# Kernel tuning notes

Measured on AMD Instinct MI355X. Metric: run time of the kernel, lower is better.

The kernel has to match this reference:

```python
import jax, jax.numpy as jnp
import numpy as np

INPUT, HIDDEN, CLASSES = 28, 128, 10

def setup_inputs() -> dict:
    key = jax.random.key(0)
    ks = jax.random.split(key, 8)
    B = 16384
    s_ih = 1.0 / np.sqrt(HIDDEN)
    return {
        "x": jax.random.normal(ks[0], (B, 1, 28, 28), dtype=jnp.float32),
        "W_ih": jax.random.uniform(ks[1], (HIDDEN, INPUT), jnp.float32, -s_ih, s_ih),
        "W_hh": jax.random.uniform(ks[2], (HIDDEN, HIDDEN), jnp.float32, -s_ih, s_ih),
        "b_ih": jax.random.uniform(ks[3], (HIDDEN,), jnp.float32, -s_ih, s_ih),
        "b_hh": jax.random.uniform(ks[4], (HIDDEN,), jnp.float32, -s_ih, s_ih),
        "W_fc": jax.random.uniform(ks[5], (CLASSES, HIDDEN), jnp.float32, -s_ih, s_ih),
        "b_fc": jax.random.uniform(ks[6], (CLASSES,), jnp.float32, -s_ih, s_ih),
    }

def reference(x, W_ih, W_hh, b_ih, b_hh, W_fc, b_fc):
    # x: [B,1,28,28] -> squeeze channel -> [B,T=28,I=28]
    xs = jnp.squeeze(x, axis=1)
    B = xs.shape[0]
    # precompute input projections for all timesteps: [B,T,H]
    xproj = jnp.einsum("bti,hi->bth", xs, W_ih) + b_ih + b_hh
    xproj_t = jnp.transpose(xproj, (1, 0, 2))  # [T,B,H]

    def step(h, xp):
        h_new = jnp.tanh(xp + h @ W_hh.T)
        return h_new, None

    h0 = jnp.zeros((B, HIDDEN), dtype=xs.dtype)
    h_last, _ = jax.lax.scan(step, h0, xproj_t)
    return h_last @ W_fc.T + b_fc  # [B, num_classes]
```

## Files before the change

### kernel.cpp

```cpp
#include <hip/hip_runtime.h>
#include <hip/hip_bf16.h>
#include <stdint.h>


typedef __attribute__((ext_vector_type(8))) short short8;
typedef __attribute__((ext_vector_type(4))) float f32x4;
typedef __attribute__((ext_vector_type(4))) uint32_t u32x4;

union Frag { short8 s; uint32_t u[4]; u32x4 v; };

#define MFMA16(a,b,c) __builtin_amdgcn_mfma_f32_16x16x32_bf16((a),(b),(c),0,0,0)

__device__ __forceinline__ uint32_t pk2(float a, float b){
    union { __hip_bfloat162 h; uint32_t u; } cv;
    cv.h = __float22bfloat162_rn(make_float2(a,b));
    return cv.u;
}
__device__ __forceinline__ float lo16f(uint32_t u){ return __builtin_bit_cast(float, u<<16); }
__device__ __forceinline__ float hi16f(uint32_t u){ return __builtin_bit_cast(float, u & 0xffff0000u); }

__device__ __forceinline__ void cvt8(const f32x4& a, const f32x4& b, Frag& hi, Frag& lo){
    float v[8];
    #pragma unroll
    for(int i=0;i<4;i++){ v[i]=a[i]; v[4+i]=b[i]; }
    #pragma unroll
    for(int q=0;q<4;q++){
        uint32_t h = pk2(v[2*q], v[2*q+1]);
        hi.u[q] = h;
        lo.u[q] = pk2(v[2*q]-lo16f(h), v[2*q+1]-hi16f(h));
    }
}

__device__ __forceinline__ int piperm(int p){
    int jt = p>>4, c = p&15;
    return 32*(jt>>1) + 8*(c>>2) + 4*(jt&1) + (c&3);
}

__device__ __forceinline__ float fast_tanh(float x){
    x = fminf(fmaxf(x, -30.f), 30.f);
    float e = __expf(2.f*x);
    return (e-1.f)*__builtin_amdgcn_rcpf(e+1.f);
}

__global__ __launch_bounds__(256,2) void rnn_fused4(
    const float* __restrict__ x,   const float* __restrict__ Wih,
    const float* __restrict__ Whh, const float* __restrict__ bih,
    const float* __restrict__ bhh, const float* __restrict__ Wfc,
    const float* __restrict__ bfc, float* __restrict__ out)
{
    const int tid  = threadIdx.x;
    const int w    = tid >> 6;
    const int lane = tid & 63;
    const int g = lane>>4, c = lane&15;
    const int b0 = blockIdx.x*16;
    const f32x4 zero4 = {0.f,0.f,0.f,0.f};

    __shared__ uint32_t lds[2][2][4][64][4];

    Frag whh_h[2][4], whh_l[2][4];
    #pragma unroll
    for(int j=0;j<2;j++){
        const int row = piperm(16*(2*w+j) + c);
        const float* rp = Whh + row*128;
        #pragma unroll
        for(int kt=0;kt<4;kt++){
            f32x4 a = *(const f32x4*)(rp + kt*32 + 8*g);
            f32x4 b = *(const f32x4*)(rp + kt*32 + 8*g + 4);
            cvt8(a, b, whh_h[j][kt], whh_l[j][kt]);
        }
    }

    Frag wih_h[2], wih_l[2];
    {
        const int i1 = 8*g;
        const int i2 = (g<3) ? (8*g+4) : 24;
        #pragma unroll
        for(int j=0;j<2;j++){
            const int row = piperm(16*(2*w+j) + c);
            const float* rp = Wih + row*28;
            f32x4 a = *(const f32x4*)(rp + i1);
            f32x4 b = *(const f32x4*)(rp + i2);
            if (g==3) b = zero4;
            cvt8(a, b, wih_h[j], wih_l[j]);
        }
    }

    f32x4 biasr[2];
    #pragma unroll
    for(int j=0;j<2;j++){
        #pragma unroll
        for(int r=0;r<4;r++){
            int q = piperm(16*(2*w+j) + 4*g + r);
            biasr[j][r] = bih[q] + bhh[q];
        }
    }

    Frag bh_h[4], bh_l[4];
    #pragma unroll
    for(int kt=0;kt<4;kt++){
        #pragma unroll
        for(int q=0;q<4;q++){ bh_h[kt].u[q]=0; bh_l[kt].u[q]=0; }
    }

    const float* xrow = x + (size_t)(b0 + c)*784;
    const int o1 = 8*g;
    const int o2 = (g<3) ? (8*g+4) : 24;

    f32x4 xA = *(const f32x4*)(xrow + o1);
    f32x4 xB = *(const f32x4*)(xrow + o2);

    for(int t=0; t<28; ++t){
        f32x4 xA_n = xA, xB_n = xB;
        if (t < 27){
            xA_n = *(const f32x4*)(xrow + (t+1)*28 + o1);
            xB_n = *(const f32x4*)(xrow + (t+1)*28 + o2);
        }
        Frag bx_h, bx_l;
        {
            f32x4 b = xB;
            if (g==3) b = zero4;
            cvt8(xA, b, bx_h, bx_l);
        }
        f32x4 acc[2];
        #pragma unroll
        for(int j=0;j<2;j++){
            f32x4 a1 = MFMA16(wih_h[j].s, bx_h.s, biasr[j]);
            a1 = MFMA16(wih_l[j].s, bx_h.s, a1);
            a1 = MFMA16(wih_h[j].s, bx_l.s, a1);
            a1 = MFMA16(whh_h[j][0].s, bh_h[0].s, a1);
            a1 = MFMA16(whh_l[j][0].s, bh_h[0].s, a1);
            a1 = MFMA16(whh_h[j][0].s, bh_l[0].s, a1);
            a1 = MFMA16(whh_h[j][1].s, bh_h[1].s, a1);
            a1 = MFMA16(whh_l[j][1].s, bh_h[1].s, a1);
            a1 = MFMA16(whh_h[j][1].s, bh_l[1].s, a1);
            f32x4 a2 = MFMA16(whh_h[j][2].s, bh_h[2].s, zero4);
            a2 = MFMA16(whh_l[j][2].s, bh_h[2].s, a2);
            a2 = MFMA16(whh_h[j][2].s, bh_l[2].s, a2);
            a2 = MFMA16(whh_h[j][3].s, bh_h[3].s, a2);
            a2 = MFMA16(whh_l[j][3].s, bh_h[3].s, a2);
            a2 = MFMA16(whh_h[j][3].s, bh_l[3].s, a2);
            acc[j] = a1 + a2;
        }
        Frag nh_h, nh_l;
        #pragma unroll
        for(int j=0;j<2;j++){
            float h0 = fast_tanh(acc[j][0]);
            float h1 = fast_tanh(acc[j][1]);
            float h2 = fast_tanh(acc[j][2]);
            float h3 = fast_tanh(acc[j][3]);
            const int q0 = j*2;
            uint32_t u0 = pk2(h0,h1), u1 = pk2(h2,h3);
            nh_h.u[q0]   = u0;
            nh_h.u[q0+1] = u1;
            nh_l.u[q0]   = pk2(h0-lo16f(u0), h1-hi16f(u0));
            nh_l.u[q0+1] = pk2(h2-lo16f(u1), h3-hi16f(u1));
        }
        const int buf = t & 1;
        *(u32x4*)(&lds[buf][0][w][lane][0]) = nh_h.v;
        *(u32x4*)(&lds[buf][1][w][lane][0]) = nh_l.v;
        __syncthreads();
        #pragma unroll
        for(int kt=0;kt<4;kt++){
            bh_h[kt].v = *(const u32x4*)(&lds[buf][0][kt][lane][0]);
            bh_l[kt].v = *(const u32x4*)(&lds[buf][1][kt][lane][0]);
        }
        xA = xA_n; xB = xB_n;
    }

    if (w == 0){
        Frag wfc_h[4], wfc_l[4];
        const bool valid = (c < 10);
        const float* rp = Wfc + (valid ? c : 0)*128;
        #pragma unroll
        for(int kt=0;kt<4;kt++){
            f32x4 a = *(const f32x4*)(rp + kt*32 + 8*g);
            f32x4 b = *(const f32x4*)(rp + kt*32 + 8*g + 4);
            if(!valid){ a = zero4; b = zero4; }
            cvt8(a, b, wfc_h[kt], wfc_l[kt]);
        }
        f32x4 accf = {0.f,0.f,0.f,0.f};
        #pragma unroll
        for(int kt=0;kt<4;kt++){
            accf = MFMA16(wfc_h[kt].s, bh_h[kt].s, accf);
            accf = MFMA16(wfc_l[kt].s, bh_h[kt].s, accf);
            accf = MFMA16(wfc_h[kt].s, bh_l[kt].s, accf);
        }
        #pragma unroll
        for(int r=0;r<4;r++){
            int cls = 4*g + r;
            if (cls < 10){
                out[(size_t)(b0+c)*10 + cls] = accf[r] + bfc[cls];
            }
        }
    }
}

extern "C" void kernel_launch(void* const* d_in, const int* in_sizes, int n_in,
                              void* d_out, int out_size, void* d_ws, size_t ws_size,
                              hipStream_t stream)
{
    const float* x   = (const float*)d_in[0];
    const float* Wih = (const float*)d_in[1];
    const float* Whh = (const float*)d_in[2];
    const float* bih = (const float*)d_in[3];
    const float* bhh = (const float*)d_in[4];
    const float* Wfc = (const float*)d_in[5];
    const float* bfc = (const float*)d_in[6];
    float* out = (float*)d_out;

    const int nb = in_sizes[0] / 784;
    dim3 grid(nb/16), blk(256);
    hipLaunchKernelGGL(rnn_fused4, grid, blk, 0, stream,
                       x, Wih, Whh, bih, bhh, Wfc, bfc, out);
}
```

Baseline: 148.6 us.

## Halve waves per block, giving each wave four hidden tiles and a lighter barrier

The block shrinks from four waves to two, and each wave now computes four 16-row hidden tiles instead of two. Each wave writes two LDS slabs per step, and __syncthreads is replaced by an explicit lgkmcnt wait plus s_barrier. This aims to cut barrier and sync cost and add instruction-level parallelism across independent MFMA chains. The cost is double the serial MFMA work per wave, higher register pressure from holding twice the W_hh fragments, and half as many waves resident per CU. Smaller tweaks: tanh drops its clamp and uses 1-2/(e+1), the g==3 zeroing of x is removed because the matching W_ih entries are already zero, and the next-step x load becomes unconditional.

```diff
diff --git a/kernel.cpp b/kernel.cpp
--- a/kernel.cpp
+++ b/kernel.cpp
@@ -20,14 +20,17 @@
 __device__ __forceinline__ float hi16f(uint32_t u){ return __builtin_bit_cast(float, u & 0xffff0000u); }
 
 __device__ __forceinline__ void cvt8(const f32x4& a, const f32x4& b, Frag& hi, Frag& lo){
-    float v[8];
-    #pragma unroll
-    for(int i=0;i<4;i++){ v[i]=a[i]; v[4+i]=b[i]; }
-    #pragma unroll
-    for(int q=0;q<4;q++){
-        uint32_t h = pk2(v[2*q], v[2*q+1]);
+    #pragma unroll
+    for(int q=0;q<2;q++){
+        uint32_t h = pk2(a[2*q], a[2*q+1]);
         hi.u[q] = h;
-        lo.u[q] = pk2(v[2*q]-lo16f(h), v[2*q+1]-hi16f(h));
+        lo.u[q] = pk2(a[2*q]-lo16f(h), a[2*q+1]-hi16f(h));
+    }
+    #pragma unroll
+    for(int q=0;q<2;q++){
+        uint32_t h = pk2(b[2*q], b[2*q+1]);
+        hi.u[2+q] = h;
+        lo.u[2+q] = pk2(b[2*q]-lo16f(h), b[2*q+1]-hi16f(h));
     }
 }
 
@@ -37,12 +40,11 @@
 }
 
 __device__ __forceinline__ float fast_tanh(float x){
-    x = fminf(fmaxf(x, -30.f), 30.f);
     float e = __expf(2.f*x);
-    return (e-1.f)*__builtin_amdgcn_rcpf(e+1.f);
-}
-
-__global__ __launch_bounds__(256,2) void rnn_fused4(
+    return 1.f - 2.f*__builtin_amdgcn_rcpf(e + 1.f);
+}
+
+__global__ __launch_bounds__(128,2) void rnn_v3(
     const float* __restrict__ x,   const float* __restrict__ Wih,
     const float* __restrict__ Whh, const float* __restrict__ bih,
     const float* __restrict__ bhh, const float* __restrict__ Wfc,
@@ -57,10 +59,10 @@
 
     __shared__ uint32_t lds[2][2][4][64][4];
 
-    Frag whh_h[2][4], whh_l[2][4];
-    #pragma unroll
-    for(int j=0;j<2;j++){
-        const int row = piperm(16*(2*w+j) + c);
+    Frag whh_h[4][4], whh_l[4][4];
+    #pragma unroll
+    for(int j=0;j<4;j++){
+        const int row = piperm(16*(4*w+j) + c);
         const float* rp = Whh + row*128;
         #pragma unroll
         for(int kt=0;kt<4;kt++){
@@ -70,13 +72,13 @@
         }
     }
 
-    Frag wih_h[2], wih_l[2];
+    Frag wih_h[4], wih_l[4];
     {
         const int i1 = 8*g;
         const int i2 = (g<3) ? (8*g+4) : 24;
         #pragma unroll
-        for(int j=0;j<2;j++){
-            const int row = piperm(16*(2*w+j) + c);
+        for(int j=0;j<4;j++){
+            const int row = piperm(16*(4*w+j) + c);
             const float* rp = Wih + row*28;
             f32x4 a = *(const f32x4*)(rp + i1);
             f32x4 b = *(const f32x4*)(rp + i2);
@@ -85,12 +87,12 @@
         }
     }
 
-    f32x4 biasr[2];
-    #pragma unroll
-    for(int j=0;j<2;j++){
+    f32x4 biasr[4];
+    #pragma unroll
+    for(int j=0;j<4;j++){
         #pragma unroll
         for(int r=0;r<4;r++){
-            int q = piperm(16*(2*w+j) + 4*g + r);
+            int q = piperm(16*(4*w+j) + 4*g + r);
             biasr[j][r] = bih[q] + bhh[q];
         }
     }
@@ -110,20 +112,16 @@
     f32x4 xB = *(const f32x4*)(xrow + o2);
 
     for(int t=0; t<28; ++t){
-        f32x4 xA_n = xA, xB_n = xB;
-        if (t < 27){
-            xA_n = *(const f32x4*)(xrow + (t+1)*28 + o1);
-            xB_n = *(const f32x4*)(xrow + (t+1)*28 + o2);
-        }
+        const int tn = (t<27) ? t+1 : 27;
+        f32x4 xA_n = *(const f32x4*)(xrow + tn*28 + o1);
+        f32x4 xB_n = *(const f32x4*)(xrow + tn*28 + o2);
+
         Frag bx_h, bx_l;
-        {
-            f32x4 b = xB;
-            if (g==3) b = zero4;
-            cvt8(xA, b, bx_h, bx_l);
-        }
-        f32x4 acc[2];
-        #pragma unroll
-        for(int j=0;j<2;j++){
+        cvt8(xA, xB, bx_h, bx_l);
+
+        f32x4 acc[4];
+        #pragma unroll
+        for(int j=0;j<4;j++){
             f32x4 a1 = MFMA16(wih_h[j].s, bx_h.s, biasr[j]);
             a1 = MFMA16(wih_l[j].s, bx_h.s, a1);
             a1 = MFMA16(wih_h[j].s, bx_l.s, a1);
@@ -141,24 +139,32 @@
             a2 = MFMA16(whh_h[j][3].s, bh_l[3].s, a2);
             acc[j] = a1 + a2;
         }
-        Frag nh_h, nh_l;
-        #pragma unroll
-        for(int j=0;j<2;j++){
+
+        Frag nh_h[2], nh_l[2];
+        #pragma unroll
+        for(int j=0;j<4;j++){
             float h0 = fast_tanh(acc[j][0]);
             float h1 = fast_tanh(acc[j][1]);
             float h2 = fast_tanh(acc[j][2]);
             float h3 = fast_tanh(acc[j][3]);
-            const int q0 = j*2;
+            const int sl = j>>1;
+            const int q0 = (j&1)*2;
             uint32_t u0 = pk2(h0,h1), u1 = pk2(h2,h3);
-            nh_h.u[q0]   = u0;
-            nh_h.u[q0+1] = u1;
-            nh_l.u[q0]   = pk2(h0-lo16f(u0), h1-hi16f(u0));
-            nh_l.u[q0+1] = pk2(h2-lo16f(u1), h3-hi16f(u1));
-        }
+            nh_h[sl].u[q0]   = u0;
+            nh_h[sl].u[q0+1] = u1;
+            nh_l[sl].u[q0]   = pk2(h0-lo16f(u0), h1-hi16f(u0));
+            nh_l[sl].u[q0+1] = pk2(h2-lo16f(u1), h3-hi16f(u1));
+        }
+
         const int buf = t & 1;
-        *(u32x4*)(&lds[buf][0][w][lane][0]) = nh_h.v;
-        *(u32x4*)(&lds[buf][1][w][lane][0]) = nh_l.v;
-        __syncthreads();
+        *(u32x4*)(&lds[buf][0][2*w  ][lane][0]) = nh_h[0].v;
+        *(u32x4*)(&lds[buf][1][2*w  ][lane][0]) = nh_l[0].v;
+        *(u32x4*)(&lds[buf][0][2*w+1][lane][0]) = nh_h[1].v;
+        *(u32x4*)(&lds[buf][1][2*w+1][lane][0]) = nh_l[1].v;
+
+        asm volatile("s_waitcnt lgkmcnt(0)" ::: "memory");
+        __builtin_amdgcn_s_barrier();
+
         #pragma unroll
         for(int kt=0;kt<4;kt++){
             bh_h[kt].v = *(const u32x4*)(&lds[buf][0][kt][lane][0]);
@@ -209,7 +215,7 @@
     float* out = (float*)d_out;
 
     const int nb = in_sizes[0] / 784;
-    dim3 grid(nb/16), blk(256);
-    hipLaunchKernelGGL(rnn_fused4, grid, blk, 0, stream,
+    dim3 grid(nb/16), blk(128);
+    hipLaunchKernelGGL(rnn_v3, grid, blk, 0, stream,
                        x, Wih, Whh, bih, bhh, Wfc, bfc, out);
 }
```

Measured after the change: 146.5 us. Within noise of the previous version (-1.4%).
